# Kernel tuning notes

Measured on AMD Instinct MI355X. Metric: run time of the kernel, lower is better.

The kernel has to match this reference:

```python
import jax, jax.numpy as jnp
import numpy as np

B, L, H, E = 4, 2048, 8, 64

def setup_inputs() -> dict:
    key = jax.random.key(0)
    kq, kk, kv = jax.random.split(key, 3)
    queries = jax.random.normal(kq, (B, L, H, E), dtype=jnp.float32)
    keys = jax.random.normal(kk, (B, L, H, E), dtype=jnp.float32)
    values = jax.random.normal(kv, (B, L, H, E), dtype=jnp.float32)
    return {"queries": queries, "keys": keys, "values": values}

def reference(queries, keys, values):
    # queries/keys/values: [B, L, H, E]
    E_ = queries.shape[-1]
    scale = 1.0 / jnp.sqrt(jnp.float32(E_))
    # scores: [B, H, L, S]
    scores = jnp.einsum('blhe,bshe->bhls', queries, keys)
    Lq, S = scores.shape[-2], scores.shape[-1]
    # TriangularCausalMask: mask positions where s > l (strict upper triangle)
    causal = jnp.tril(jnp.ones((Lq, S), dtype=bool))
    scores = jnp.where(causal, scores, -jnp.inf)
    A = jax.nn.softmax(scale * scores, axis=-1)  # dropout p=0 -> identity
    V = jnp.einsum('bhls,bshd->blhd', A, values)
    return V
```

## Files before the change

### kernel.cpp

```cpp
#include <hip/hip_runtime.h>


#define Bc 4
#define Lc 2048
#define Hc 8
#define Ec 64
#define TILEB 8192
#define NKV 32
#define BHB ((size_t)NKV * TILEB)
#define WSV ((size_t)32 * BHB)

using f32x4 = __attribute__((ext_vector_type(4))) float;
using f16x8 = __attribute__((ext_vector_type(8))) _Float16;
using f16x4 = __attribute__((ext_vector_type(4))) _Float16;
using hf16x2 = __fp16 __attribute__((ext_vector_type(2)));
using u32x4 = __attribute__((ext_vector_type(4))) unsigned int;

static __device__ __forceinline__ unsigned int pk2(float lo, float hi) {
    union { hf16x2 h; unsigned int u; } c;
    c.h = __builtin_amdgcn_cvt_pkrtz(lo, hi);
    return c.u;
}
static __device__ __forceinline__ u32x4 nt16(const void* p) {
    return __builtin_nontemporal_load((const u32x4*)p);
}

__global__ __launch_bounds__(256)
void prep_kernel(const float* __restrict__ K, const float* __restrict__ V,
                 char* __restrict__ ws)
{
    __shared__ char kst[64 * 128];
    __shared__ char vst[64 * 144];
    __shared__ char vtt[64 * 128];

    const int bid = blockIdx.x;
    const int bh = bid >> 5, kt = bid & 31;
    const int b = bh >> 3, h = bh & 7;
    const int tid = threadIdx.x;
    const size_t base = (size_t)b * Lc * Hc * Ec + (size_t)h * Ec;

    {
        const int r = tid >> 2, q4 = tid & 3, c0 = 16 * q4;
        const float* kp = K + base + (size_t)(kt * 64 + r) * 512 + c0;
        const float* vp = V + base + (size_t)(kt * 64 + r) * 512 + c0;
        unsigned int wk[8], wv[8];
        #pragma unroll
        for (int i = 0; i < 4; ++i) {
            union { u32x4 v; float f[4]; } fk, fv;
            fk.v = nt16(kp + 4 * i);
            fv.v = nt16(vp + 4 * i);
            wk[2*i]   = pk2(fk.f[0], fk.f[1]); wk[2*i+1] = pk2(fk.f[2], fk.f[3]);
            wv[2*i]   = pk2(fv.f[0], fv.f[1]); wv[2*i+1] = pk2(fv.f[2], fv.f[3]);
        }
        *(uint4*)(kst + r * 128 + 2 * c0)      = *(uint4*)&wk[0];
        *(uint4*)(kst + r * 128 + 2 * c0 + 16) = *(uint4*)&wk[4];
        *(uint4*)(vst + r * 144 + 2 * c0)      = *(uint4*)&wv[0];
        *(uint4*)(vst + r * 144 + 2 * c0 + 16) = *(uint4*)&wv[4];
    }
    __syncthreads();
    {
        const int e = tid >> 2, kq = tid & 3, kv0 = 16 * kq;
        unsigned int w[8];
        #pragma unroll
        for (int i = 0; i < 8; ++i) {
            unsigned int lo = *(const unsigned short*)(vst + (kv0 + 2*i)     * 144 + 2*e);
            unsigned int hi = *(const unsigned short*)(vst + (kv0 + 2*i + 1) * 144 + 2*e);
            w[i] = lo | (hi << 16);
        }
        *(uint4*)(vtt + e * 128 + 2 * kv0)      = *(uint4*)&w[0];
        *(uint4*)(vtt + e * 128 + 2 * kv0 + 16) = *(uint4*)&w[4];
    }
    __syncthreads();
    {
        const int lane = tid & 63, qq = tid >> 6;
        const int l15 = lane & 15, l4 = lane >> 4;
        char* ko = ws + (size_t)bh * BHB + (size_t)kt * TILEB;
        char* vo = ws + WSV + (size_t)bh * BHB + (size_t)kt * TILEB;
        uint4 k0 = *(const uint4*)(kst + (16 * qq + l15) * 128 + 16 * l4);
        uint4 k1 = *(const uint4*)(kst + (16 * qq + l15) * 128 + 64 + 16 * l4);
        *(uint4*)(ko + (2 * qq)     * 1024 + lane * 16) = k0;
        *(uint4*)(ko + (2 * qq + 1) * 1024 + lane * 16) = k1;
        unsigned long long vv[4];
        #pragma unroll
        for (int c = 0; c < 4; ++c)
            vv[c] = *(const unsigned long long*)(vtt + (16 * c + l15) * 128 + 32 * qq + 8 * l4);
        uint4 v01, v23;
        v01.x = (unsigned)vv[0]; v01.y = (unsigned)(vv[0] >> 32);
        v01.z = (unsigned)vv[1]; v01.w = (unsigned)(vv[1] >> 32);
        v23.x = (unsigned)vv[2]; v23.y = (unsigned)(vv[2] >> 32);
        v23.z = (unsigned)vv[3]; v23.w = (unsigned)(vv[3] >> 32);
        *(uint4*)(vo + (2 * qq)     * 1024 + lane * 16) = v01;
        *(uint4*)(vo + (2 * qq + 1) * 1024 + lane * 16) = v23;
    }
}

__global__ __launch_bounds__(256, 3)
void fa_fwd_kernel(const float* __restrict__ Q, const char* __restrict__ ws,
                   float* __restrict__ Out)
{
    const int bid = blockIdx.x;
    const int qi  = bid >> 5;
    const int bh  = bid & 31;
    const int qt  = 31 - qi;
    const int b   = bh >> 3, h = bh & 7;

    const int tid  = threadIdx.x;
    const int wid  = tid >> 6;
    const int lane = tid & 63;
    const int l15  = lane & 15, l4 = lane >> 4;

    const size_t base = (size_t)b * Lc * Hc * Ec + (size_t)h * Ec;
    const char* kimg = ws + (size_t)bh * BHB + lane * 16;
    const char* vimg = ws + WSV + (size_t)bh * BHB + lane * 16;
    const float SL2E = 0.125f * 1.44269504088896340736f;

    f16x4 ones;
    {
        const _Float16 ov = (_Float16)((l15 == 0) ? 1.0f : 0.0f);
        ones[0] = ov; ones[1] = ov; ones[2] = ov; ones[3] = ov;
    }

    const int qrow0 = qt * 64 + 16 * wid;
    const int mysteps = qt + 1;

    f16x8 qa0, qa1;
    {
        const float* qpr = Q + base + (size_t)(qrow0 + l15) * 512 + 8 * l4;
        union { u32x4 v; float f[4]; } f0, f1, f2, f3;
        f0.v = nt16(qpr);      f1.v = nt16(qpr + 4);
        f2.v = nt16(qpr + 32); f3.v = nt16(qpr + 36);
        union { f16x8 v; unsigned int u[4]; } pk;
        pk.u[0] = pk2(f0.f[0] * SL2E, f0.f[1] * SL2E);
        pk.u[1] = pk2(f0.f[2] * SL2E, f0.f[3] * SL2E);
        pk.u[2] = pk2(f1.f[0] * SL2E, f1.f[1] * SL2E);
        pk.u[3] = pk2(f1.f[2] * SL2E, f1.f[3] * SL2E);
        qa0 = pk.v;
        pk.u[0] = pk2(f2.f[0] * SL2E, f2.f[1] * SL2E);
        pk.u[1] = pk2(f2.f[2] * SL2E, f2.f[3] * SL2E);
        pk.u[2] = pk2(f3.f[0] * SL2E, f3.f[1] * SL2E);
        pk.u[3] = pk2(f3.f[2] * SL2E, f3.f[3] * SL2E);
        qa1 = pk.v;
    }

    f32x4 o[4] = {};
    f32x4 ol = {};
    float m_run = -1e30f;

    uint4 kf[8], vf[8];
    #pragma unroll
    for (int j = 0; j < 8; ++j) kf[j] = *(const uint4*)(kimg + j * 1024);
    #pragma unroll
    for (int j = 0; j < 8; ++j) vf[j] = *(const uint4*)(vimg + j * 1024);

    #pragma unroll 1
    for (int kt = 0; kt < mysteps; ++kt) {
        f32x4 s[4];
        #pragma unroll
        for (int n = 0; n < 4; ++n) {
            union { uint4 u; f16x8 h; } a0, a1;
            a0.u = kf[2 * n]; a1.u = kf[2 * n + 1];
            f32x4 z = {0.f, 0.f, 0.f, 0.f};
            z = __builtin_amdgcn_mfma_f32_16x16x32_f16(a0.h, qa0, z, 0, 0, 0);
            z = __builtin_amdgcn_mfma_f32_16x16x32_f16(a1.h, qa1, z, 0, 0, 0);
            s[n] = z;
        }

        if (kt + 1 < mysteps) {
            const char* kp = kimg + (size_t)(kt + 1) * TILEB;
            #pragma unroll
            for (int j = 0; j < 8; ++j) kf[j] = *(const uint4*)(kp + j * 1024);
        }

        if (kt == mysteps - 1) {
            const int q_g = qrow0 + l15;
            #pragma unroll
            for (int n = 0; n < 4; ++n) {
                #pragma unroll
                for (int r2 = 0; r2 < 4; ++r2) {
                    const int kv_g = kt * 64 + 16 * n + 4 * l4 + r2;
                    if (kv_g > q_g) s[n][r2] = -1e30f;
                }
            }
        }

        float a0 = fmaxf(s[0][0], s[0][1]), a1 = fmaxf(s[0][2], s[0][3]);
        float a2 = fmaxf(s[1][0], s[1][1]), a3 = fmaxf(s[1][2], s[1][3]);
        float a4 = fmaxf(s[2][0], s[2][1]), a5 = fmaxf(s[2][2], s[2][3]);
        float a6 = fmaxf(s[3][0], s[3][1]), a7 = fmaxf(s[3][2], s[3][3]);
        float pmax = fmaxf(fmaxf(fmaxf(a0, a1), fmaxf(a2, a3)),
                           fmaxf(fmaxf(a4, a5), fmaxf(a6, a7)));
        pmax = fmaxf(pmax, __shfl_xor(pmax, 16, 64));
        pmax = fmaxf(pmax, __shfl_xor(pmax, 32, 64));

        if (!__all(pmax - m_run <= 8.0f)) {
            const float m_new = fmaxf(m_run, pmax);
            const float fac = __builtin_exp2f(m_run - m_new);
            m_run = m_new;
            float fr[4];
            #pragma unroll
            for (int r2 = 0; r2 < 4; ++r2) fr[r2] = __shfl(fac, 4 * l4 + r2, 64);
            #pragma unroll
            for (int c = 0; c < 4; ++c)
                #pragma unroll
                for (int r2 = 0; r2 < 4; ++r2) o[c][r2] *= fr[r2];
            #pragma unroll
            for (int r2 = 0; r2 < 4; ++r2) ol[r2] *= fr[r2];
        }

        unsigned int ph[4][2];
        #pragma unroll
        for (int n = 0; n < 4; ++n) {
            float p0 = __builtin_exp2f(s[n][0] - m_run);
            float p1 = __builtin_exp2f(s[n][1] - m_run);
            float p2 = __builtin_exp2f(s[n][2] - m_run);
            float p3 = __builtin_exp2f(s[n][3] - m_run);
            ph[n][0] = pk2(p0, p1);
            ph[n][1] = pk2(p2, p3);
        }

        #pragma unroll
        for (int m = 0; m < 4; ++m) {
            union { uint4 u; f16x4 h[2]; } w0, w1;
            w0.u = vf[2 * m]; w1.u = vf[2 * m + 1];
            union { f16x4 h; unsigned int u[2]; } pa;
            pa.u[0] = ph[m][0]; pa.u[1] = ph[m][1];
            ol   = __builtin_amdgcn_mfma_f32_16x16x16f16(pa.h, ones,    ol,   0, 0, 0);
            o[0] = __builtin_amdgcn_mfma_f32_16x16x16f16(pa.h, w0.h[0], o[0], 0, 0, 0);
            o[1] = __builtin_amdgcn_mfma_f32_16x16x16f16(pa.h, w0.h[1], o[1], 0, 0, 0);
            o[2] = __builtin_amdgcn_mfma_f32_16x16x16f16(pa.h, w1.h[0], o[2], 0, 0, 0);
            o[3] = __builtin_amdgcn_mfma_f32_16x16x16f16(pa.h, w1.h[1], o[3], 0, 0, 0);
        }

        if (kt + 1 < mysteps) {
            const char* vp2 = vimg + (size_t)(kt + 1) * TILEB;
            #pragma unroll
            for (int j = 0; j < 8; ++j) vf[j] = *(const uint4*)(vp2 + j * 1024);
        }
    }

    float ir[4];
    #pragma unroll
    for (int r2 = 0; r2 < 4; ++r2) {
        const float iv = 1.0f / ol[r2];
        ir[r2] = __shfl(iv, 16 * l4, 64);
    }
    float* op = Out + base;
    #pragma unroll
    for (int c = 0; c < 4; ++c)
        #pragma unroll
        for (int r2 = 0; r2 < 4; ++r2)
            __builtin_nontemporal_store(o[c][r2] * ir[r2],
                op + (size_t)(qrow0 + 4 * l4 + r2) * 512 + 16 * c + l15);
}

extern "C" void kernel_launch(void* const* d_in, const int* in_sizes, int n_in,
                              void* d_out, int out_size, void* d_ws, size_t ws_size,
                              hipStream_t stream) {
    const float* Q = (const float*)d_in[0];
    const float* K = (const float*)d_in[1];
    const float* V = (const float*)d_in[2];
    float* O = (float*)d_out;
    char* ws = (char*)d_ws;
    hipLaunchKernelGGL(prep_kernel, dim3(32 * NKV), dim3(256), 0, stream, K, V, ws);
    hipLaunchKernelGGL(fa_fwd_kernel, dim3(32 * 32), dim3(256), 0, stream, Q, ws, O);
}
```

Before: 66.08 us.

## Interleave per-subtile softmax with PV MFMA and compute row sums in registers

The 64-key tile loop now processes four 16-key subtiles one at a time: QK MFMA, masking, online max update, exp, then PV MFMA, with the next tile's K/V fragments prefetched per subtile instead of in bulk. The row-sum MFMA against a ones vector is replaced by a scalar lsum accumulated in registers and reduced with shuffles at the end. The running max starts at 8 and rescaling is triggered per subtile when any score exceeds it. The aim is to cut MFMA work and overlap loads with compute, but per-subtile branching and rescaling may occur more often. The unconditional prefetch on the last step reloads the current tile.

```diff
diff --git a/kernel.cpp b/kernel.cpp
--- a/kernel.cpp
+++ b/kernel.cpp
@@ -113,12 +113,6 @@
     const char* kimg = ws + (size_t)bh * BHB + lane * 16;
     const char* vimg = ws + WSV + (size_t)bh * BHB + lane * 16;
     const float SL2E = 0.125f * 1.44269504088896340736f;
-
-    f16x4 ones;
-    {
-        const _Float16 ov = (_Float16)((l15 == 0) ? 1.0f : 0.0f);
-        ones[0] = ov; ones[1] = ov; ones[2] = ov; ones[3] = ov;
-    }
 
     const int qrow0 = qt * 64 + 16 * wid;
     const int mysteps = qt + 1;
@@ -143,8 +137,8 @@
     }
 
     f32x4 o[4] = {};
-    f32x4 ol = {};
-    float m_run = -1e30f;
+    float lsum = 0.f;
+    float m_run = 8.0f;
 
     uint4 kf[8], vf[8];
     #pragma unroll
@@ -154,96 +148,76 @@
 
     #pragma unroll 1
     for (int kt = 0; kt < mysteps; ++kt) {
-        f32x4 s[4];
-        #pragma unroll
-        for (int n = 0; n < 4; ++n) {
+        const int nxt = (kt + 1 < mysteps) ? kt + 1 : kt;
+        const char* kp = kimg + (size_t)nxt * TILEB;
+        const char* vp = vimg + (size_t)nxt * TILEB;
+        const bool last = (kt == mysteps - 1);
+
+        #pragma unroll
+        for (int m = 0; m < 4; ++m) {
             union { uint4 u; f16x8 h; } a0, a1;
-            a0.u = kf[2 * n]; a1.u = kf[2 * n + 1];
-            f32x4 z = {0.f, 0.f, 0.f, 0.f};
-            z = __builtin_amdgcn_mfma_f32_16x16x32_f16(a0.h, qa0, z, 0, 0, 0);
-            z = __builtin_amdgcn_mfma_f32_16x16x32_f16(a1.h, qa1, z, 0, 0, 0);
-            s[n] = z;
-        }
-
-        if (kt + 1 < mysteps) {
-            const char* kp = kimg + (size_t)(kt + 1) * TILEB;
-            #pragma unroll
-            for (int j = 0; j < 8; ++j) kf[j] = *(const uint4*)(kp + j * 1024);
-        }
-
-        if (kt == mysteps - 1) {
-            const int q_g = qrow0 + l15;
-            #pragma unroll
-            for (int n = 0; n < 4; ++n) {
+            a0.u = kf[2 * m]; a1.u = kf[2 * m + 1];
+            f32x4 s = {0.f, 0.f, 0.f, 0.f};
+            s = __builtin_amdgcn_mfma_f32_16x16x32_f16(a0.h, qa0, s, 0, 0, 0);
+            s = __builtin_amdgcn_mfma_f32_16x16x32_f16(a1.h, qa1, s, 0, 0, 0);
+
+            kf[2 * m]     = *(const uint4*)(kp + (2 * m)     * 1024);
+            kf[2 * m + 1] = *(const uint4*)(kp + (2 * m + 1) * 1024);
+
+            if (last) {
+                const int q_g = qrow0 + l15;
                 #pragma unroll
                 for (int r2 = 0; r2 < 4; ++r2) {
-                    const int kv_g = kt * 64 + 16 * n + 4 * l4 + r2;
-                    if (kv_g > q_g) s[n][r2] = -1e30f;
+                    const int kv_g = kt * 64 + 16 * m + 4 * l4 + r2;
+                    if (kv_g > q_g) s[r2] = -1e30f;
                 }
             }
-        }
-
-        float a0 = fmaxf(s[0][0], s[0][1]), a1 = fmaxf(s[0][2], s[0][3]);
-        float a2 = fmaxf(s[1][0], s[1][1]), a3 = fmaxf(s[1][2], s[1][3]);
-        float a4 = fmaxf(s[2][0], s[2][1]), a5 = fmaxf(s[2][2], s[2][3]);
-        float a6 = fmaxf(s[3][0], s[3][1]), a7 = fmaxf(s[3][2], s[3][3]);
-        float pmax = fmaxf(fmaxf(fmaxf(a0, a1), fmaxf(a2, a3)),
-                           fmaxf(fmaxf(a4, a5), fmaxf(a6, a7)));
-        pmax = fmaxf(pmax, __shfl_xor(pmax, 16, 64));
-        pmax = fmaxf(pmax, __shfl_xor(pmax, 32, 64));
-
-        if (!__all(pmax - m_run <= 8.0f)) {
-            const float m_new = fmaxf(m_run, pmax);
-            const float fac = __builtin_exp2f(m_run - m_new);
-            m_run = m_new;
-            float fr[4];
-            #pragma unroll
-            for (int r2 = 0; r2 < 4; ++r2) fr[r2] = __shfl(fac, 4 * l4 + r2, 64);
-            #pragma unroll
-            for (int c = 0; c < 4; ++c)
+
+            const float cmax = fmaxf(fmaxf(s[0], s[1]), fmaxf(s[2], s[3]));
+            if (__any(cmax > m_run)) {
+                float pm = cmax;
+                pm = fmaxf(pm, __shfl_xor(pm, 16, 64));
+                pm = fmaxf(pm, __shfl_xor(pm, 32, 64));
+                const float m_new = fmaxf(m_run, pm);
+                const float fac = __builtin_exp2f(m_run - m_new);
+                m_run = m_new;
+                lsum *= fac;
+                float fr[4];
                 #pragma unroll
-                for (int r2 = 0; r2 < 4; ++r2) o[c][r2] *= fr[r2];
-            #pragma unroll
-            for (int r2 = 0; r2 < 4; ++r2) ol[r2] *= fr[r2];
-        }
-
-        unsigned int ph[4][2];
-        #pragma unroll
-        for (int n = 0; n < 4; ++n) {
-            float p0 = __builtin_exp2f(s[n][0] - m_run);
-            float p1 = __builtin_exp2f(s[n][1] - m_run);
-            float p2 = __builtin_exp2f(s[n][2] - m_run);
-            float p3 = __builtin_exp2f(s[n][3] - m_run);
-            ph[n][0] = pk2(p0, p1);
-            ph[n][1] = pk2(p2, p3);
-        }
-
-        #pragma unroll
-        for (int m = 0; m < 4; ++m) {
+                for (int r2 = 0; r2 < 4; ++r2) fr[r2] = __shfl(fac, 4 * l4 + r2, 64);
+                #pragma unroll
+                for (int c = 0; c < 4; ++c)
+                    #pragma unroll
+                    for (int r2 = 0; r2 < 4; ++r2) o[c][r2] *= fr[r2];
+            }
+
+            const float p0 = __builtin_exp2f(s[0] - m_run);
+            const float p1 = __builtin_exp2f(s[1] - m_run);
+            const float p2 = __builtin_exp2f(s[2] - m_run);
+            const float p3 = __builtin_exp2f(s[3] - m_run);
+            lsum += (p0 + p1) + (p2 + p3);
+            union { f16x4 h; unsigned int u[2]; } pa;
+            pa.u[0] = pk2(p0, p1);
+            pa.u[1] = pk2(p2, p3);
+
             union { uint4 u; f16x4 h[2]; } w0, w1;
             w0.u = vf[2 * m]; w1.u = vf[2 * m + 1];
-            union { f16x4 h; unsigned int u[2]; } pa;
-            pa.u[0] = ph[m][0]; pa.u[1] = ph[m][1];
-            ol   = __builtin_amdgcn_mfma_f32_16x16x16f16(pa.h, ones,    ol,   0, 0, 0);
             o[0] = __builtin_amdgcn_mfma_f32_16x16x16f16(pa.h, w0.h[0], o[0], 0, 0, 0);
             o[1] = __builtin_amdgcn_mfma_f32_16x16x16f16(pa.h, w0.h[1], o[1], 0, 0, 0);
             o[2] = __builtin_amdgcn_mfma_f32_16x16x16f16(pa.h, w1.h[0], o[2], 0, 0, 0);
             o[3] = __builtin_amdgcn_mfma_f32_16x16x16f16(pa.h, w1.h[1], o[3], 0, 0, 0);
+
+            vf[2 * m]     = *(const uint4*)(vp + (2 * m)     * 1024);
+            vf[2 * m + 1] = *(const uint4*)(vp + (2 * m + 1) * 1024);
         }
-
-        if (kt + 1 < mysteps) {
-            const char* vp2 = vimg + (size_t)(kt + 1) * TILEB;
-            #pragma unroll
-            for (int j = 0; j < 8; ++j) vf[j] = *(const uint4*)(vp2 + j * 1024);
-        }
-    }
-
+    }
+
+    lsum += __shfl_xor(lsum, 16, 64);
+    lsum += __shfl_xor(lsum, 32, 64);
+    const float inv = 1.0f / lsum;
     float ir[4];
     #pragma unroll
-    for (int r2 = 0; r2 < 4; ++r2) {
-        const float iv = 1.0f / ol[r2];
-        ir[r2] = __shfl(iv, 16 * l4, 64);
-    }
+    for (int r2 = 0; r2 < 4; ++r2) ir[r2] = __shfl(inv, 4 * l4 + r2, 64);
     float* op = Out + base;
     #pragma unroll
     for (int c = 0; c < 4; ++c)
```

Result: slower. 67.83 us (+2.7%).
